# Kernel tuning notes

Hardware: AMD Instinct MI355X
Metric: run time of the kernel (lower is better)

## Reference

```python
import jax, jax.numpy as jnp
import numpy as np

N, M = 8192, 128
EPS = 1e-4


def setup_inputs() -> dict:
    key = jax.random.key(0)
    k1, k2, k3 = jax.random.split(key, 3)
    out1 = jax.random.normal(k1, (N, M), dtype=jnp.float32)
    out2 = jax.random.normal(k2, (N, M), dtype=jnp.float32)
    label = jax.random.uniform(k3, (N, N), dtype=jnp.float32)
    return {"out1": out1, "out2": out2, "label": label}


def _dir_loss(a, b, mob):
    # pairwise_inner_product(a, b) in the torch code equals b @ a.T:
    # inner[i, j] = <b[i], a[j]>
    scores = jnp.einsum('im,jm->ij', b, a)          # [n, n]
    phat = jax.nn.softmax(scores, axis=-1)
    return jnp.sum(-mob * jnp.log(phat + EPS))


def reference(out1, out2, label):
    loss = _dir_loss(out1, out2, label)
    loss = loss + _dir_loss(out2, out1, label.T)
    return loss
```

## Files before the change

kernel.cpp:

```cpp
#include <hip/hip_runtime.h>
#include <hip/hip_bf16.h>

#define NN 8192
#define MM 128
#define EPSF 1e-4f
#define SHIFT 30.0f

typedef __bf16 bf16x8 __attribute__((ext_vector_type(8)));
typedef __bf16 bf16x4 __attribute__((ext_vector_type(4)));
typedef float floatx4 __attribute__((ext_vector_type(4)));

__global__ void convert_kernel(const float* __restrict__ in0,
                               const float* __restrict__ in1,
                               __bf16* __restrict__ o0,
                               __bf16* __restrict__ o1) {
    const float* in = blockIdx.y ? in1 : in0;
    __bf16* out = blockIdx.y ? o1 : o0;
    int i = (blockIdx.x * blockDim.x + threadIdx.x) * 4;
    float4 v = *reinterpret_cast<const float4*>(in + i);
    bf16x4 o = { (__bf16)v.x, (__bf16)v.y, (__bf16)v.z, (__bf16)v.w };
    *reinterpret_cast<bf16x4*>(out + i) = o;
}

#define LOAD_A(dst, ptr)                                                   \
    do {                                                                   \
        dst[0] = *reinterpret_cast<const bf16x8*>((ptr) + 0);              \
        dst[1] = *reinterpret_cast<const bf16x8*>((ptr) + 32);             \
        dst[2] = *reinterpret_cast<const bf16x8*>((ptr) + 64);             \
        dst[3] = *reinterpret_cast<const bf16x8*>((ptr) + 96);             \
    } while (0)

__global__ __launch_bounds__(256)
void rowsum_kernel(const __bf16* __restrict__ X2, const __bf16* __restrict__ X1,
                   float* __restrict__ sums) {
    const int dir = blockIdx.z;
    const __bf16* A = dir ? X1 : X2;
    const __bf16* B = dir ? X2 : X1;
    float* sum = sums + dir * NN;

    const int tid = threadIdx.x;
    const int w = tid >> 6, lane = tid & 63, q = lane >> 4, ln = lane & 15;
    const int i0 = blockIdx.y * 128 + w * 32;
    const int jbase = blockIdx.x * 1024;

    bf16x8 a[2][4];
    #pragma unroll
    for (int rg = 0; rg < 2; ++rg) {
        const __bf16* ar = A + (size_t)(i0 + rg * 16 + ln) * MM + q * 8;
        LOAD_A(a[rg], ar);
    }

    float p[2][4] = {{0.f, 0.f, 0.f, 0.f}, {0.f, 0.f, 0.f, 0.f}};

    for (int js = 0; js < 16; ++js) {
        const int j0 = jbase + js * 64;
        bf16x8 b[4][4];
        #pragma unroll
        for (int cg = 0; cg < 4; ++cg) {
            const __bf16* br = B + (size_t)(j0 + cg * 16 + ln) * MM + q * 8;
            LOAD_A(b[cg], br);
        }
        #pragma unroll
        for (int cg = 0; cg < 4; ++cg) {
            floatx4 acc0 = {0.f, 0.f, 0.f, 0.f};
            floatx4 acc1 = {0.f, 0.f, 0.f, 0.f};
            #pragma unroll
            for (int k = 0; k < 4; ++k) {
                acc0 = __builtin_amdgcn_mfma_f32_16x16x32_bf16(a[0][k], b[cg][k], acc0, 0, 0, 0);
                acc1 = __builtin_amdgcn_mfma_f32_16x16x32_bf16(a[1][k], b[cg][k], acc1, 0, 0, 0);
            }
            #pragma unroll
            for (int r = 0; r < 4; ++r) {
                p[0][r] += __expf(acc0[r] - SHIFT);
                p[1][r] += __expf(acc1[r] - SHIFT);
            }
        }
    }

    #pragma unroll
    for (int m = 1; m <= 8; m <<= 1) {
        #pragma unroll
        for (int rg = 0; rg < 2; ++rg)
            #pragma unroll
            for (int r = 0; r < 4; ++r)
                p[rg][r] += __shfl_xor(p[rg][r], m);
    }
    if (ln == 0) {
        #pragma unroll
        for (int rg = 0; rg < 2; ++rg)
            #pragma unroll
            for (int r = 0; r < 4; ++r)
                atomicAdd(&sum[i0 + rg * 16 + q * 4 + r], p[rg][r]);
    }
}

__global__ void recip_kernel(const float* __restrict__ s, float* __restrict__ r) {
    int i = blockIdx.x * 256 + threadIdx.x;
    r[i] = 1.0f / s[i];
}

__global__ __launch_bounds__(256)
void loss_kernel(const __bf16* __restrict__ A, const __bf16* __restrict__ B,
                 const float* __restrict__ lrowR, const float* __restrict__ lcolR,
                 const float* __restrict__ label, float* __restrict__ out) {
    const int tid = threadIdx.x;
    const int w = tid >> 6, lane = tid & 63, q = lane >> 4, ln = lane & 15;
    const int i0 = blockIdx.y * 128 + w * 32;
    const int jbase = blockIdx.x * 256;

    bf16x8 a[2][4];
    float rl[2];
    const float* labp[2];
    #pragma unroll
    for (int rg = 0; rg < 2; ++rg) {
        const int row = i0 + rg * 16 + ln;
        LOAD_A(a[rg], A + (size_t)row * MM + q * 8);
        rl[rg] = lrowR[row];
        labp[rg] = label + (size_t)row * NN;
    }

    float lacc = 0.f;
    #pragma unroll
    for (int js = 0; js < 4; ++js) {
        const int j0 = jbase + js * 64;
        floatx4 rc[4], lb[2][4];
        #pragma unroll
        for (int cg = 0; cg < 4; ++cg) {
            const int c4 = j0 + cg * 16 + q * 4;
            rc[cg] = *reinterpret_cast<const floatx4*>(&lcolR[c4]);
            lb[0][cg] = *reinterpret_cast<const floatx4*>(&labp[0][c4]);
            lb[1][cg] = *reinterpret_cast<const floatx4*>(&labp[1][c4]);
        }
        #pragma unroll
        for (int cg = 0; cg < 4; ++cg) {
            const __bf16* br = B + (size_t)(j0 + cg * 16 + ln) * MM + q * 8;
            bf16x8 b[4];
            LOAD_A(b, br);
            floatx4 acc0 = {0.f, 0.f, 0.f, 0.f};
            floatx4 acc1 = {0.f, 0.f, 0.f, 0.f};
            #pragma unroll
            for (int k = 0; k < 4; ++k) {
                acc0 = __builtin_amdgcn_mfma_f32_16x16x32_bf16(b[k], a[0][k], acc0, 0, 0, 0);
                acc1 = __builtin_amdgcn_mfma_f32_16x16x32_bf16(b[k], a[1][k], acc1, 0, 0, 0);
            }
            #pragma unroll
            for (int r = 0; r < 4; ++r) {
                float e0 = __expf(acc0[r] - SHIFT);
                float t0 = __logf(fmaf(e0, rl[0], EPSF) * fmaf(e0, rc[cg][r], EPSF));
                lacc = fmaf(lb[0][cg][r], t0, lacc);
                float e1 = __expf(acc1[r] - SHIFT);
                float t1 = __logf(fmaf(e1, rl[1], EPSF) * fmaf(e1, rc[cg][r], EPSF));
                lacc = fmaf(lb[1][cg][r], t1, lacc);
            }
        }
    }

    #pragma unroll
    for (int m = 1; m <= 32; m <<= 1) lacc += __shfl_xor(lacc, m);
    __shared__ float red[4];
    if (lane == 0) red[w] = lacc;
    __syncthreads();
    if (tid == 0) atomicAdd(out, -((red[0] + red[1]) + (red[2] + red[3])));
}

extern "C" void kernel_launch(void* const* d_in, const int* in_sizes, int n_in,
                              void* d_out, int out_size, void* d_ws, size_t ws_size,
                              hipStream_t stream) {
    const float* out1 = (const float*)d_in[0];
    const float* out2 = (const float*)d_in[1];
    const float* label = (const float*)d_in[2];

    char* ws = (char*)d_ws;
    __bf16* out1b = (__bf16*)ws;
    __bf16* out2b = (__bf16*)(ws + (size_t)(2 << 20));
    float* sums   = (float*)(ws + (size_t)(4 << 20));
    float* recips = sums + 2 * NN;

    hipMemsetAsync(sums, 0, 2 * NN * sizeof(float), stream);
    hipMemsetAsync(d_out, 0, sizeof(float), stream);

    convert_kernel<<<dim3(1024, 2), 256, 0, stream>>>(out1, out2, out1b, out2b);

    rowsum_kernel<<<dim3(8, 64, 2), 256, 0, stream>>>(out2b, out1b, sums);
    recip_kernel<<<dim3(64), 256, 0, stream>>>(sums, recips);

    loss_kernel<<<dim3(32, 64), 256, 0, stream>>>(out2b, out1b,
                                                  recips,
                                                  recips + NN,
                                                  label, (float*)d_out);
}
```

Measured before the change: 518.2 us.

## Compute row and column exp-sums from one score pass instead of two GEMMs

The row-sum kernel used to compute the score matrix twice, once per direction, to get softmax denominators. The second direction's scores are just the transpose, so one pass now produces both. Each tile's exponentials are summed along rows in registers and along columns with cross-lane shuffles plus atomic adds into the second sums array. This roughly halves the MFMA and exp work in that stage, at the cost of many more global atomics for the column sums. The constant shift is also folded into the accumulator's initial value, saving a subtract per element.

```diff
diff --git a/kernel.cpp b/kernel.cpp
--- a/kernel.cpp
+++ b/kernel.cpp
@@ -31,67 +31,65 @@
     } while (0)
 
 __global__ __launch_bounds__(256)
-void rowsum_kernel(const __bf16* __restrict__ X2, const __bf16* __restrict__ X1,
-                   float* __restrict__ sums) {
-    const int dir = blockIdx.z;
-    const __bf16* A = dir ? X1 : X2;
-    const __bf16* B = dir ? X2 : X1;
-    float* sum = sums + dir * NN;
-
+void sums_kernel(const __bf16* __restrict__ A, const __bf16* __restrict__ B,
+                 float* __restrict__ sums) {
     const int tid = threadIdx.x;
     const int w = tid >> 6, lane = tid & 63, q = lane >> 4, ln = lane & 15;
     const int i0 = blockIdx.y * 128 + w * 32;
-    const int jbase = blockIdx.x * 1024;
+    const int jbase = blockIdx.x * 512;
+
+    const floatx4 accInit = {-SHIFT, -SHIFT, -SHIFT, -SHIFT};
 
     bf16x8 a[2][4];
     #pragma unroll
-    for (int rg = 0; rg < 2; ++rg) {
-        const __bf16* ar = A + (size_t)(i0 + rg * 16 + ln) * MM + q * 8;
-        LOAD_A(a[rg], ar);
-    }
+    for (int rg = 0; rg < 2; ++rg)
+        LOAD_A(a[rg], A + (size_t)(i0 + rg * 16 + ln) * MM + q * 8);
 
     float p[2][4] = {{0.f, 0.f, 0.f, 0.f}, {0.f, 0.f, 0.f, 0.f}};
 
-    for (int js = 0; js < 16; ++js) {
+    for (int js = 0; js < 8; ++js) {
         const int j0 = jbase + js * 64;
         bf16x8 b[4][4];
         #pragma unroll
-        for (int cg = 0; cg < 4; ++cg) {
-            const __bf16* br = B + (size_t)(j0 + cg * 16 + ln) * MM + q * 8;
-            LOAD_A(b[cg], br);
-        }
+        for (int cg = 0; cg < 4; ++cg)
+            LOAD_A(b[cg], B + (size_t)(j0 + cg * 16 + ln) * MM + q * 8);
         #pragma unroll
         for (int cg = 0; cg < 4; ++cg) {
-            floatx4 acc0 = {0.f, 0.f, 0.f, 0.f};
-            floatx4 acc1 = {0.f, 0.f, 0.f, 0.f};
+            floatx4 acc0 = accInit, acc1 = accInit;
             #pragma unroll
             for (int k = 0; k < 4; ++k) {
                 acc0 = __builtin_amdgcn_mfma_f32_16x16x32_bf16(a[0][k], b[cg][k], acc0, 0, 0, 0);
                 acc1 = __builtin_amdgcn_mfma_f32_16x16x32_bf16(a[1][k], b[cg][k], acc1, 0, 0, 0);
             }
+            float e0[4], e1[4];
             #pragma unroll
             for (int r = 0; r < 4; ++r) {
-                p[0][r] += __expf(acc0[r] - SHIFT);
-                p[1][r] += __expf(acc1[r] - SHIFT);
+                e0[r] = __expf(acc0[r]);
+                e1[r] = __expf(acc1[r]);
+                p[0][r] += e0[r];
+                p[1][r] += e1[r];
             }
+            float c = ((e0[0] + e0[1]) + (e0[2] + e0[3])) +
+                      ((e1[0] + e1[1]) + (e1[2] + e1[3]));
+            c += __shfl_xor(c, 16);
+            c += __shfl_xor(c, 32);
+            if (q == 0) atomicAdd(&sums[NN + j0 + cg * 16 + ln], c);
         }
     }
 
     #pragma unroll
-    for (int m = 1; m <= 8; m <<= 1) {
+    for (int m = 1; m <= 8; m <<= 1)
         #pragma unroll
         for (int rg = 0; rg < 2; ++rg)
             #pragma unroll
             for (int r = 0; r < 4; ++r)
                 p[rg][r] += __shfl_xor(p[rg][r], m);
-    }
-    if (ln == 0) {
+    if (ln == 0)
         #pragma unroll
         for (int rg = 0; rg < 2; ++rg)
             #pragma unroll
             for (int r = 0; r < 4; ++r)
-                atomicAdd(&sum[i0 + rg * 16 + q * 4 + r], p[rg][r]);
-    }
+                atomicAdd(&sums[i0 + rg * 16 + q * 4 + r], p[rg][r]);
 }
 
 __global__ void recip_kernel(const float* __restrict__ s, float* __restrict__ r) {
@@ -107,6 +105,8 @@
     const int w = tid >> 6, lane = tid & 63, q = lane >> 4, ln = lane & 15;
     const int i0 = blockIdx.y * 128 + w * 32;
     const int jbase = blockIdx.x * 256;
+
+    const floatx4 accInit = {-SHIFT, -SHIFT, -SHIFT, -SHIFT};
 
     bf16x8 a[2][4];
     float rl[2];
@@ -136,8 +136,7 @@
             const __bf16* br = B + (size_t)(j0 + cg * 16 + ln) * MM + q * 8;
             bf16x8 b[4];
             LOAD_A(b, br);
-            floatx4 acc0 = {0.f, 0.f, 0.f, 0.f};
-            floatx4 acc1 = {0.f, 0.f, 0.f, 0.f};
+            floatx4 acc0 = accInit, acc1 = accInit;
             #pragma unroll
             for (int k = 0; k < 4; ++k) {
                 acc0 = __builtin_amdgcn_mfma_f32_16x16x32_bf16(b[k], a[0][k], acc0, 0, 0, 0);
@@ -145,10 +144,10 @@
             }
             #pragma unroll
             for (int r = 0; r < 4; ++r) {
-                float e0 = __expf(acc0[r] - SHIFT);
+                float e0 = __expf(acc0[r]);
                 float t0 = __logf(fmaf(e0, rl[0], EPSF) * fmaf(e0, rc[cg][r], EPSF));
                 lacc = fmaf(lb[0][cg][r], t0, lacc);
-                float e1 = __expf(acc1[r] - SHIFT);
+                float e1 = __expf(acc1[r]);
                 float t1 = __logf(fmaf(e1, rl[1], EPSF) * fmaf(e1, rc[cg][r], EPSF));
                 lacc = fmaf(lb[1][cg][r], t1, lacc);
             }
@@ -181,7 +180,7 @@
 
     convert_kernel<<<dim3(1024, 2), 256, 0, stream>>>(out1, out2, out1b, out2b);
 
-    rowsum_kernel<<<dim3(8, 64, 2), 256, 0, stream>>>(out2b, out1b, sums);
+    sums_kernel<<<dim3(16, 64), 256, 0, stream>>>(out2b, out1b, sums);
     recip_kernel<<<dim3(64), 256, 0, stream>>>(sums, recips);
 
     loss_kernel<<<dim3(32, 64), 256, 0, stream>>>(out2b, out1b,
```

After: 459.1 us. 11.4% less time.
